# Kernel tuning notes

Hardware: AMD Instinct MI355X
Metric: run time of the kernel (lower is better)

## Reference

```python
import jax, jax.numpy as jnp
import numpy as np

DIM = 128
B, LQ, LK = 8, 2048, 2048


def setup_inputs() -> dict:
    key = jax.random.key(0)
    k1, k2, k3 = jax.random.split(key, 3)
    output = jax.random.normal(k1, (B, LQ, DIM), dtype=jnp.float32)
    context = jax.random.normal(k2, (B, LK, DIM), dtype=jnp.float32)
    mask = jax.random.randint(k3, (B, LQ, LK), 0, 2).astype(jnp.bool_)
    return {"output": output, "context": context, "mask": mask}


def reference(output, context, mask):
    temperature = jnp.asarray(np.power(DIM, 0.5), dtype=output.dtype)
    # scores: [B, Lq, Lk]
    attn = jnp.einsum('bqd,bkd->bqk', output, context) / temperature
    attn = jnp.where(mask, -jnp.inf, attn)
    out_attn = jax.nn.log_softmax(attn, axis=-1)
    p = jax.nn.softmax(attn, axis=-1)
    # dropout is identity in eval/reference mode
    out = jnp.einsum('bqk,bkd->bqd', p, context)
    return (out, out_attn)
```

## Files before the change

kernel.cpp:

```cpp
#include <hip/hip_runtime.h>
#include <cstdint>


#define DIMV 128
constexpr int BB = 8;
constexpr int LQ = 2048;
constexpr int LK = 2048;
constexpr float QSCALE = 0.08838834764831843f;

typedef _Float16 half8 __attribute__((ext_vector_type(8)));
typedef _Float16 half4v __attribute__((ext_vector_type(4)));
typedef float float4v __attribute__((ext_vector_type(4)));

__global__ __launch_bounds__(256) void prep_kernel(const float* __restrict__ q,
                                                   const float* __restrict__ ctx,
                                                   _Float16* __restrict__ Qf,
                                                   _Float16* __restrict__ Kf,
                                                   _Float16* __restrict__ Vf) {
    __shared__ float tile[32][132];
    const int tid  = threadIdx.x;
    const int mode = blockIdx.x >> 9;
    const int t    = blockIdx.x & 511;
    const int b    = t >> 6;
    const int r0   = (t & 63) * 32;
    const float4* s4 = (const float4*)((mode == 0 ? q : ctx) + ((size_t)b * 2048 + r0) * DIMV);
    for (int v = 0; v < 4; v++) {
        int off = tid + v * 256;
        float4 f = s4[off];
        int row = off >> 5, c4 = (off & 31) * 4;
        tile[row][c4 + 0] = f.x; tile[row][c4 + 1] = f.y;
        tile[row][c4 + 2] = f.z; tile[row][c4 + 3] = f.w;
    }
    __syncthreads();
    if (mode < 2) {
        const float qs = (mode == 0) ? QSCALE : 1.0f;
        _Float16* dst = (mode == 0 ? Qf : Kf) + (size_t)b * (2048 * DIMV);
        for (int c = 0; c < 2; c++) {
            int chunk = tid + c * 256;
            int t2 = chunk >> 8, kk = (chunk >> 6) & 3, lane = chunk & 63;
            int quad = lane >> 4, l16 = lane & 15;
            int r = t2 * 16 + l16, d0 = kk * 32 + quad * 8;
            half8 h;
            for (int e = 0; e < 8; e++) h[e] = (_Float16)(tile[r][d0 + e] * qs);
            size_t tl = (size_t)(r0 >> 4) + t2;
            *(half8*)(dst + ((tl * 4 + kk) * 64 + lane) * 8) = h;
        }
    } else {
        _Float16* dst = Vf + (size_t)b * (2048 * DIMV);
        const int kt0 = r0 >> 4;
        for (int c = 0; c < 2; c++) {
            int chunk = tid + c * 256;
            int ktl = chunk >> 8, dp = (chunk >> 6) & 3, ln = chunk & 63;
            int qd = ln >> 4, s16 = ln & 15;
            half8 h;
            for (int e = 0; e < 4; e++) {
                h[e]     = (_Float16)tile[ktl * 16 + qd * 4 + e][(2 * dp) * 16 + s16];
                h[e + 4] = (_Float16)tile[ktl * 16 + qd * 4 + e][(2 * dp + 1) * 16 + s16];
            }
            *(half8*)(dst + ((((size_t)(kt0 + ktl)) * 4 + dp) * 64 + ln) * 8) = h;
        }
    }
}

__global__ __launch_bounds__(256, 2)
void attn_kernel(const unsigned char* __restrict__ mask,
                 const _Float16* __restrict__ Qf, const _Float16* __restrict__ Kf,
                 const _Float16* __restrict__ Vf,
                 float* __restrict__ out, float* __restrict__ out_attn) {
    __shared__ __attribute__((aligned(16))) float pvsum[32][132];
    __shared__ float redm[4][32], redl[4][32], swf[4][32];
    __shared__ float mcl32[32], rls32[32];

    const int tid  = threadIdx.x;
    const int wave = tid >> 6;
    const int lane = tid & 63;
    const int l16  = lane & 15;
    const int quad = lane >> 4;

    const int b  = blockIdx.x & 7;
    const int qg = blockIdx.x >> 3;
    const int q0 = qg * 32;

    const _Float16* Qb = Qf + (size_t)b * (2048 * DIMV);
    const _Float16* Kb = Kf + (size_t)b * (2048 * DIMV);
    const _Float16* Vb = Vf + (size_t)b * (2048 * DIMV);

    half8 qfrag[2][4];
#pragma unroll
    for (int sub = 0; sub < 2; sub++) {
        const size_t tq = (size_t)qg * 2 + sub;
#pragma unroll
        for (int kk = 0; kk < 4; kk++)
            qfrag[sub][kk] = *(const half8*)(Qb + ((tq * 4 + kk) * 64 + lane) * 8);
    }

    const unsigned char* mrow0 = mask + ((size_t)b * LQ + q0 + l16) * LK + wave * 512 + quad * 4;

    const _Float16* kstrip = Kb + (size_t)wave * 32 * 2048;
    const _Float16* vstrip = Vb + (size_t)wave * 32 * 2048;

    const float NEGINF = -__builtin_inff();
    float m0r = -1e30f, m1r = -1e30f;
    float l0r = 0.f, l1r = 0.f;
    float4v oacc[2][8];
#pragma unroll
    for (int sub = 0; sub < 2; sub++)
#pragma unroll
        for (int dt = 0; dt < 8; dt++) oacc[sub][dt] = (float4v){0.f, 0.f, 0.f, 0.f};

    half8 kfb[2][4], vvb[2][4];
    uint32_t mvb[2][2];
    {
#pragma unroll
        for (int kk = 0; kk < 4; kk++) kfb[0][kk] = *(const half8*)(kstrip + (kk * 64 + lane) * 8);
#pragma unroll
        for (int dp = 0; dp < 4; dp++) vvb[0][dp] = *(const half8*)(vstrip + (dp * 64 + lane) * 8);
#pragma unroll
        for (int s = 0; s < 2; s++) mvb[0][s] = *(const uint32_t*)(mrow0 + (size_t)s * 16 * LK);
    }

#pragma unroll 2
    for (int ct = 0; ct < 32; ++ct) {
        const int cur = ct & 1, nxt = cur ^ 1;
        const int cn  = (ct + 1) & 31;
        {
            const _Float16* kp = kstrip + (size_t)cn * 2048;
            const _Float16* vp = vstrip + (size_t)cn * 2048;
#pragma unroll
            for (int kk = 0; kk < 4; kk++) kfb[nxt][kk] = *(const half8*)(kp + (kk * 64 + lane) * 8);
#pragma unroll
            for (int dp = 0; dp < 4; dp++) vvb[nxt][dp] = *(const half8*)(vp + (dp * 64 + lane) * 8);
#pragma unroll
            for (int s = 0; s < 2; s++)
                mvb[nxt][s] = *(const uint32_t*)(mrow0 + (size_t)s * 16 * LK + cn * 16);
        }
        __builtin_amdgcn_sched_barrier(0);

#pragma unroll
        for (int sub = 0; sub < 2; sub++) {
            float4v st = (float4v){0.f, 0.f, 0.f, 0.f};
            __builtin_amdgcn_s_setprio(1);
#pragma unroll
            for (int kk = 0; kk < 4; kk++)
                st = __builtin_amdgcn_mfma_f32_16x16x32_f16(kfb[cur][kk], qfrag[sub][kk], st, 0, 0, 0);
            __builtin_amdgcn_s_setprio(0);
            const uint32_t mv = mvb[cur][sub];
            float& m = sub ? m1r : m0r;
            float& l = sub ? l1r : l0r;
            float sv[4];
#pragma unroll
            for (int r = 0; r < 4; r++) {
                float v = st[r];
                if ((mv >> (8 * r)) & 0xffu) v = NEGINF;
                sv[r] = v;
            }
            float tmax = fmaxf(fmaxf(sv[0], sv[1]), fmaxf(sv[2], sv[3]));
            tmax = fmaxf(tmax, __shfl_xor(tmax, 16));
            tmax = fmaxf(tmax, __shfl_xor(tmax, 32));
            const bool upd = tmax > m + 3.0f;
            if (__any(upd)) {
                const float mnew = upd ? tmax : m;
                const float sc = __expf(m - mnew);
                float scr[4];
#pragma unroll
                for (int r = 0; r < 4; r++) scr[r] = __shfl(sc, quad * 4 + r);
                l *= sc;
#pragma unroll
                for (int dt = 0; dt < 8; dt++)
#pragma unroll
                    for (int r = 0; r < 4; r++) oacc[sub][dt][r] *= scr[r];
                m = mnew;
            }
            half4v pa;
            float pp[4];
#pragma unroll
            for (int r = 0; r < 4; r++) {
                pp[r] = __expf(sv[r] - m);
                pa[r] = (_Float16)pp[r];
            }
            __builtin_amdgcn_s_setprio(1);
#pragma unroll
            for (int dp = 0; dp < 4; dp++) {
                half4v vlo = __builtin_shufflevector(vvb[cur][dp], vvb[cur][dp], 0, 1, 2, 3);
                half4v vhi = __builtin_shufflevector(vvb[cur][dp], vvb[cur][dp], 4, 5, 6, 7);
                oacc[sub][2 * dp]     = __builtin_amdgcn_mfma_f32_16x16x16f16(pa, vlo, oacc[sub][2 * dp],     0, 0, 0);
                oacc[sub][2 * dp + 1] = __builtin_amdgcn_mfma_f32_16x16x16f16(pa, vhi, oacc[sub][2 * dp + 1], 0, 0, 0);
            }
            __builtin_amdgcn_s_setprio(0);
            float psum = (pp[0] + pp[1]) + (pp[2] + pp[3]);
            psum += __shfl_xor(psum, 16);
            psum += __shfl_xor(psum, 32);
            l += psum;
        }
    }

    if (quad == 0) {
        redm[wave][l16]      = m0r;  redm[wave][16 + l16] = m1r;
        redl[wave][l16]      = l0r;  redl[wave][16 + l16] = l1r;
    }
    half8 kf2[2][4];
    uint32_t mv2[2][2];
#pragma unroll
    for (int kk = 0; kk < 4; kk++) kf2[0][kk] = *(const half8*)(kstrip + (kk * 64 + lane) * 8);
#pragma unroll
    for (int s = 0; s < 2; s++) mv2[0][s] = *(const uint32_t*)(mrow0 + (size_t)s * 16 * LK);
    __syncthreads();
    if (tid < 32) {
        float mm[4], ll[4];
#pragma unroll
        for (int p = 0; p < 4; p++) { mm[p] = redm[p][tid]; ll[p] = redl[p][tid]; }
        const float M = fmaxf(fmaxf(mm[0], mm[1]), fmaxf(mm[2], mm[3]));
        float L = 0.f;
#pragma unroll
        for (int p = 0; p < 4; p++) {
            const float e = __expf(mm[p] - M);
            swf[p][tid] = e;
            L += e * ll[p];
        }
        mcl32[tid] = M + __logf(L);
        rls32[tid] = 1.0f / L;
    }
    __syncthreads();

    for (int rnd = 0; rnd < 4; ++rnd) {
        if (wave == rnd) {
#pragma unroll
            for (int sub = 0; sub < 2; sub++)
#pragma unroll
                for (int r = 0; r < 4; r++) {
                    const int row = sub * 16 + quad * 4 + r;
                    const float sc = swf[wave][row];
#pragma unroll
                    for (int dt = 0; dt < 8; dt++) {
                        const float v = oacc[sub][dt][r] * sc;
                        if (rnd == 0) pvsum[row][dt * 16 + l16] = v;
                        else          pvsum[row][dt * 16 + l16] += v;
                    }
                }
        }
        __syncthreads();
    }

    {
        const int row = tid >> 3;
        const int c0  = (tid & 7) * 16;
        const float rcl = rls32[row];
        float* op = out + ((size_t)b * LQ + q0 + row) * DIMV + c0;
#pragma unroll
        for (int h = 0; h < 4; h++) {
            float4v a = *(const float4v*)&pvsum[row][c0 + h * 4];
            float4v v;
#pragma unroll
            for (int j = 0; j < 4; j++) v[j] = a[j] * rcl;
            *(float4v*)(op + h * 4) = v;
        }
    }

    const float mc0 = mcl32[l16];
    const float mc1 = mcl32[16 + l16];
    float* oa0 = out_attn + ((size_t)b * LQ + q0 + l16) * LK + wave * 512 + quad * 4;
#pragma unroll 2
    for (int ct = 0; ct < 32; ++ct) {
        const int cur = ct & 1, nxt = cur ^ 1;
        const int cn  = (ct + 1) & 31;
        {
            const _Float16* kp = kstrip + (size_t)cn * 2048;
#pragma unroll
            for (int kk = 0; kk < 4; kk++) kf2[nxt][kk] = *(const half8*)(kp + (kk * 64 + lane) * 8);
#pragma unroll
            for (int s = 0; s < 2; s++)
                mv2[nxt][s] = *(const uint32_t*)(mrow0 + (size_t)s * 16 * LK + cn * 16);
        }
        __builtin_amdgcn_sched_barrier(0);

#pragma unroll
        for (int sub = 0; sub < 2; sub++) {
            float4v st = (float4v){0.f, 0.f, 0.f, 0.f};
            __builtin_amdgcn_s_setprio(1);
#pragma unroll
            for (int kk = 0; kk < 4; kk++)
                st = __builtin_amdgcn_mfma_f32_16x16x32_f16(kf2[cur][kk], qfrag[sub][kk], st, 0, 0, 0);
            __builtin_amdgcn_s_setprio(0);
            const uint32_t mv = mv2[cur][sub];
            const float mc = sub ? mc1 : mc0;
            float4v o;
#pragma unroll
            for (int r = 0; r < 4; r++) {
                float lp = st[r] - mc;
                if ((mv >> (8 * r)) & 0xffu) lp = -1.0e30f;
                o[r] = fmaxf(lp, -1.0e30f);
            }
            *(float4v*)(oa0 + (size_t)sub * 16 * LK + ct * 16) = o;
        }
    }
}

extern "C" void kernel_launch(void* const* d_in, const int* in_sizes, int n_in,
                              void* d_out, int out_size, void* d_ws, size_t ws_size,
                              hipStream_t stream) {
    const float* q_f32 = (const float*)d_in[0];
    const float* c_f32 = (const float*)d_in[1];
    const unsigned char* mask = (const unsigned char*)d_in[2];

    float* out      = (float*)d_out;
    float* out_attn = out + (size_t)BB * LQ * DIMV;

    _Float16* Qf = (_Float16*)d_ws;
    _Float16* Kf = Qf + (size_t)BB * LQ * DIMV;
    _Float16* Vf = Kf + (size_t)BB * LK * DIMV;

    prep_kernel<<<1536, 256, 0, stream>>>(q_f32, c_f32, Qf, Kf, Vf);
    attn_kernel<<<BB * (LQ / 32), 256, 0, stream>>>(mask, Qf, Kf, Vf, out, out_attn);
}
```

Before: 277.1 us.

## Split key range across 8 waves per block and prepack mask bits once

```diff
diff --git a/kernel.cpp b/kernel.cpp
--- a/kernel.cpp
+++ b/kernel.cpp
@@ -62,13 +62,13 @@
     }
 }
 
-__global__ __launch_bounds__(256, 2)
+__global__ __launch_bounds__(512, 4)
 void attn_kernel(const unsigned char* __restrict__ mask,
                  const _Float16* __restrict__ Qf, const _Float16* __restrict__ Kf,
                  const _Float16* __restrict__ Vf,
                  float* __restrict__ out, float* __restrict__ out_attn) {
-    __shared__ __attribute__((aligned(16))) float pvsum[32][132];
-    __shared__ float redm[4][32], redl[4][32], swf[4][32];
+    __shared__ __attribute__((aligned(16))) float pvsum[2][32][132];
+    __shared__ float redm[8][32], redl[8][32], swf[8][32];
     __shared__ float mcl32[32], rls32[32];
 
     const int tid  = threadIdx.x;
@@ -94,10 +94,23 @@
             qfrag[sub][kk] = *(const half8*)(Qb + ((tq * 4 + kk) * 64 + lane) * 8);
     }
 
-    const unsigned char* mrow0 = mask + ((size_t)b * LQ + q0 + l16) * LK + wave * 512 + quad * 4;
-
-    const _Float16* kstrip = Kb + (size_t)wave * 32 * 2048;
-    const _Float16* vstrip = Vb + (size_t)wave * 32 * 2048;
+    const unsigned char* mrow0 = mask + ((size_t)b * LQ + q0 + l16) * LK + wave * 256 + quad * 4;
+    uint64_t mpack[2];
+#pragma unroll
+    for (int sub = 0; sub < 2; sub++) {
+        uint64_t pk = 0;
+#pragma unroll
+        for (int ct = 0; ct < 16; ct++) {
+            uint32_t w = *(const uint32_t*)(mrow0 + (size_t)sub * 16 * LK + ct * 16);
+            w |= w >> 4; w |= w >> 2; w |= w >> 1;
+            uint32_t nib = (w & 1u) | ((w >> 7) & 2u) | ((w >> 14) & 4u) | ((w >> 21) & 8u);
+            pk |= (uint64_t)nib << (ct * 4);
+        }
+        mpack[sub] = pk;
+    }
+
+    const _Float16* kstrip = Kb + (size_t)wave * 16 * 2048;
+    const _Float16* vstrip = Vb + (size_t)wave * 16 * 2048;
 
     const float NEGINF = -__builtin_inff();
     float m0r = -1e30f, m1r = -1e30f;
@@ -109,20 +122,17 @@
         for (int dt = 0; dt < 8; dt++) oacc[sub][dt] = (float4v){0.f, 0.f, 0.f, 0.f};
 
     half8 kfb[2][4], vvb[2][4];
-    uint32_t mvb[2][2];
     {
 #pragma unroll
         for (int kk = 0; kk < 4; kk++) kfb[0][kk] = *(const half8*)(kstrip + (kk * 64 + lane) * 8);
 #pragma unroll
         for (int dp = 0; dp < 4; dp++) vvb[0][dp] = *(const half8*)(vstrip + (dp * 64 + lane) * 8);
-#pragma unroll
-        for (int s = 0; s < 2; s++) mvb[0][s] = *(const uint32_t*)(mrow0 + (size_t)s * 16 * LK);
     }
 
 #pragma unroll 2
-    for (int ct = 0; ct < 32; ++ct) {
+    for (int ct = 0; ct < 16; ++ct) {
         const int cur = ct & 1, nxt = cur ^ 1;
-        const int cn  = (ct + 1) & 31;
+        const int cn  = (ct + 1) & 15;
         {
             const _Float16* kp = kstrip + (size_t)cn * 2048;
             const _Float16* vp = vstrip + (size_t)cn * 2048;
@@ -130,9 +140,6 @@
             for (int kk = 0; kk < 4; kk++) kfb[nxt][kk] = *(const half8*)(kp + (kk * 64 + lane) * 8);
 #pragma unroll
             for (int dp = 0; dp < 4; dp++) vvb[nxt][dp] = *(const half8*)(vp + (dp * 64 + lane) * 8);
-#pragma unroll
-            for (int s = 0; s < 2; s++)
-                mvb[nxt][s] = *(const uint32_t*)(mrow0 + (size_t)s * 16 * LK + cn * 16);
         }
         __builtin_amdgcn_sched_barrier(0);
 
@@ -144,14 +151,14 @@
             for (int kk = 0; kk < 4; kk++)
                 st = __builtin_amdgcn_mfma_f32_16x16x32_f16(kfb[cur][kk], qfrag[sub][kk], st, 0, 0, 0);
             __builtin_amdgcn_s_setprio(0);
-            const uint32_t mv = mvb[cur][sub];
+            const uint32_t mb = (uint32_t)(mpack[sub] >> (ct * 4)) & 0xFu;
             float& m = sub ? m1r : m0r;
             float& l = sub ? l1r : l0r;
             float sv[4];
 #pragma unroll
             for (int r = 0; r < 4; r++) {
                 float v = st[r];
-                if ((mv >> (8 * r)) & 0xffu) v = NEGINF;
+                if ((mb >> r) & 1u) v = NEGINF;
                 sv[r] = v;
             }
             float tmax = fmaxf(fmaxf(sv[0], sv[1]), fmaxf(sv[2], sv[3]));
@@ -199,20 +206,19 @@
         redl[wave][l16]      = l0r;  redl[wave][16 + l16] = l1r;
     }
     half8 kf2[2][4];
-    uint32_t mv2[2][2];
 #pragma unroll
     for (int kk = 0; kk < 4; kk++) kf2[0][kk] = *(const half8*)(kstrip + (kk * 64 + lane) * 8);
-#pragma unroll
-    for (int s = 0; s < 2; s++) mv2[0][s] = *(const uint32_t*)(mrow0 + (size_t)s * 16 * LK);
     __syncthreads();
     if (tid < 32) {
-        float mm[4], ll[4];
-#pragma unroll
-        for (int p = 0; p < 4; p++) { mm[p] = redm[p][tid]; ll[p] = redl[p][tid]; }
-        const float M = fmaxf(fmaxf(mm[0], mm[1]), fmaxf(mm[2], mm[3]));
+        float mm[8], ll[8];
+#pragma unroll
+        for (int p = 0; p < 8; p++) { mm[p] = redm[p][tid]; ll[p] = redl[p][tid]; }
+        float M = mm[0];
+#pragma unroll
+        for (int p = 1; p < 8; p++) M = fmaxf(M, mm[p]);
         float L = 0.f;
 #pragma unroll
-        for (int p = 0; p < 4; p++) {
+        for (int p = 0; p < 8; p++) {
             const float e = __expf(mm[p] - M);
             swf[p][tid] = e;
             L += e * ll[p];
@@ -223,7 +229,8 @@
     __syncthreads();
 
     for (int rnd = 0; rnd < 4; ++rnd) {
-        if (wave == rnd) {
+        if ((wave & 3) == rnd) {
+            const int bf = wave >> 2;
 #pragma unroll
             for (int sub = 0; sub < 2; sub++)
 #pragma unroll
@@ -233,8 +240,8 @@
 #pragma unroll
                     for (int dt = 0; dt < 8; dt++) {
                         const float v = oacc[sub][dt][r] * sc;
-                        if (rnd == 0) pvsum[row][dt * 16 + l16] = v;
-                        else          pvsum[row][dt * 16 + l16] += v;
+                        if (rnd == 0) pvsum[bf][row][dt * 16 + l16] = v;
+                        else          pvsum[bf][row][dt * 16 + l16] += v;
                     }
                 }
         }
@@ -242,34 +249,32 @@
     }
 
     {
-        const int row = tid >> 3;
-        const int c0  = (tid & 7) * 16;
+        const int row = tid >> 4;
+        const int c0  = (tid & 15) * 8;
         const float rcl = rls32[row];
         float* op = out + ((size_t)b * LQ + q0 + row) * DIMV + c0;
 #pragma unroll
-        for (int h = 0; h < 4; h++) {
-            float4v a = *(const float4v*)&pvsum[row][c0 + h * 4];
+        for (int h = 0; h < 2; h++) {
+            float4v a0 = *(const float4v*)&pvsum[0][row][c0 + h * 4];
+            float4v a1 = *(const float4v*)&pvsum[1][row][c0 + h * 4];
             float4v v;
 #pragma unroll
-            for (int j = 0; j < 4; j++) v[j] = a[j] * rcl;
+            for (int j = 0; j < 4; j++) v[j] = (a0[j] + a1[j]) * rcl;
             *(float4v*)(op + h * 4) = v;
         }
     }
 
     const float mc0 = mcl32[l16];
     const float mc1 = mcl32[16 + l16];
-    float* oa0 = out_attn + ((size_t)b * LQ + q0 + l16) * LK + wave * 512 + quad * 4;
+    float* oa0 = out_attn + ((size_t)b * LQ + q0 + l16) * LK + wave * 256 + quad * 4;
 #pragma unroll 2
-    for (int ct = 0; ct < 32; ++ct) {
+    for (int ct = 0; ct < 16; ++ct) {
         const int cur = ct & 1, nxt = cur ^ 1;
-        const int cn  = (ct + 1) & 31;
+        const int cn  = (ct + 1) & 15;
         {
             const _Float16* kp = kstrip + (size_t)cn * 2048;
 #pragma unroll
             for (int kk = 0; kk < 4; kk++) kf2[nxt][kk] = *(const half8*)(kp + (kk * 64 + lane) * 8);
-#pragma unroll
-            for (int s = 0; s < 2; s++)
-                mv2[nxt][s] = *(const uint32_t*)(mrow0 + (size_t)s * 16 * LK + cn * 16);
         }
         __builtin_amdgcn_sched_barrier(0);
 
@@ -281,13 +286,13 @@
             for (int kk = 0; kk < 4; kk++)
                 st = __builtin_amdgcn_mfma_f32_16x16x32_f16(kf2[cur][kk], qfrag[sub][kk], st, 0, 0, 0);
             __builtin_amdgcn_s_setprio(0);
-            const uint32_t mv = mv2[cur][sub];
+            const uint32_t mb = (uint32_t)(mpack[sub] >> (ct * 4)) & 0xFu;
             const float mc = sub ? mc1 : mc0;
             float4v o;
 #pragma unroll
             for (int r = 0; r < 4; r++) {
                 float lp = st[r] - mc;
-                if ((mv >> (8 * r)) & 0xffu) lp = -1.0e30f;
+                if ((mb >> r) & 1u) lp = -1.0e30f;
                 o[r] = fmaxf(lp, -1.0e30f);
             }
             *(float4v*)(oa0 + (size_t)sub * 16 * LK + ct * 16) = o;
@@ -310,5 +315,5 @@
     _Float16* Vf = Kf + (size_t)BB * LK * DIMV;
 
     prep_kernel<<<1536, 256, 0, stream>>>(q_f32, c_f32, Qf, Kf, Vf);
-    attn_kernel<<<BB * (LQ / 32), 256, 0, stream>>>(mask, Qf, Kf, Vf, out, out_attn);
+    attn_kernel<<<BB * (LQ / 32), 512, 0, stream>>>(mask, Qf, Kf, Vf, out, out_attn);
 }
```

Result: slower. 463.8 us (+67.4%).
